# Kernel tuning notes

Measured on AMD Instinct MI355X. Metric: run time of the kernel, lower is better.

The kernel has to match this reference:

```python
import jax, jax.numpy as jnp
import numpy as np
from jax import lax

C = 64      # embed_dim
DI = 128    # d_inner (expand=2)
N = 16      # d_state
RK = 4      # dt_rank = ceil(C/16)
K = 4       # scan directions
NB = 8      # total VSS blocks (4 stages x 2)


def conv2d(x, w, b, stride=1, pad=1, groups=1):
    y = lax.conv_general_dilated(x, w, (stride, stride), [(pad, pad), (pad, pad)],
                                 dimension_numbers=('NCHW', 'OIHW', 'NCHW'),
                                 feature_group_count=groups)
    return y + b[None, :, None, None]


def ln2d(x, g, b, eps=1e-6):
    xt = x.transpose(0, 2, 3, 1)
    mu = xt.mean(-1, keepdims=True)
    var = ((xt - mu) ** 2).mean(-1, keepdims=True)
    y = (xt - mu) / jnp.sqrt(var + eps) * g + b
    return y.transpose(0, 3, 1, 2)


def selective_scan(u, delta, A, Bm, Cm, D):
    # u, delta: (B,K,d,L); A: (K,d,n); Bm, Cm: (B,K,n,L); D: (K,d)
    dA = jnp.exp(delta[..., None] * A[None, :, :, None, :])               # (B,K,d,L,n)
    dBu = delta[..., None] * Bm.transpose(0, 1, 3, 2)[:, :, None] * u[..., None]

    def comb(c1, c2):
        a1, b1 = c1
        a2, b2 = c2
        return a2 * a1, a2 * b1 + b2

    _, h = lax.associative_scan(comb, (dA, dBu), axis=3)                  # (B,K,d,L,n)
    y = jnp.einsum('bkdln,bkln->bkdl', h, Cm.transpose(0, 1, 3, 2))
    return y + D[None, :, :, None] * u


def vss_block(x, lg, lb, inw, cw, cb, xpw, dtw, dtb, a_log, dp, ong, onb, outw):
    B, _, H, W = x.shape
    L = H * W
    h = ln2d(x, lg, lb)
    xz = jnp.einsum('bchw,ce->behw', h, inw)                              # (B,2*DI,H,W)
    xc, z = xz[:, :DI], xz[:, DI:]
    xc = jax.nn.silu(conv2d(xc, cw, cb, groups=DI))                       # depthwise 3x3
    x1 = xc.reshape(B, DI, L)                                             # row-major
    x2 = xc.transpose(0, 1, 3, 2).reshape(B, DI, L)                       # col-major
    xs = jnp.stack([x1, x2, x1[..., ::-1], x2[..., ::-1]], axis=1)        # (B,K,DI,L)
    xdbl = jnp.einsum('bkdl,krd->bkrl', xs, xpw)
    dts, Bs, Cs = xdbl[:, :, :RK], xdbl[:, :, RK:RK + N], xdbl[:, :, RK + N:]
    delta = jax.nn.softplus(jnp.einsum('bkrl,kdr->bkdl', dts, dtw) + dtb[None, :, :, None])
    A = -jnp.exp(a_log)
    ys = selective_scan(xs, delta, A, Bs, Cs, dp)                         # (B,K,DI,L)
    y = (ys[:, 0].reshape(B, DI, H, W)
         + ys[:, 1].reshape(B, DI, W, H).transpose(0, 1, 3, 2)
         + ys[:, 2, :, ::-1].reshape(B, DI, H, W)
         + ys[:, 3, :, ::-1].reshape(B, DI, W, H).transpose(0, 1, 3, 2))
    yt = y.transpose(0, 2, 3, 1)
    mu = yt.mean(-1, keepdims=True)
    var = ((yt - mu) ** 2).mean(-1, keepdims=True)
    yt = (yt - mu) / jnp.sqrt(var + 1e-6) * ong + onb
    yt = yt * jax.nn.silu(z.transpose(0, 2, 3, 1))
    out = jnp.einsum('bhwd,dc->bhwc', yt, outw).transpose(0, 3, 1, 2)
    return x + out


def setup_inputs() -> dict:
    key = jax.random.key(0)
    ks = jax.random.split(key, 16)
    nrm = lambda k, s, sc=0.02: jax.random.normal(k, s, jnp.float32) * sc
    return dict(
        E0=jax.random.uniform(ks[0], (1, 1, 256, 256), jnp.float32),
        pe_w=nrm(ks[1], (C, 1, 4, 4), 0.1),
        pe_b=jnp.zeros((C,), jnp.float32),
        pe_lg=jnp.ones((C,), jnp.float32),
        pe_lb=jnp.zeros((C,), jnp.float32),
        ln_g=jnp.ones((NB, C), jnp.float32),
        ln_b=jnp.zeros((NB, C), jnp.float32),
        in_w=nrm(ks[2], (NB, C, 2 * DI)),
        cv_w=nrm(ks[3], (NB, DI, 1, 3, 3), 0.1),
        cv_b=jnp.zeros((NB, DI), jnp.float32),
        xp_w=nrm(ks[4], (NB, K, RK + 2 * N, DI)),
        dt_w=nrm(ks[5], (NB, K, DI, RK)),
        dt_b=nrm(ks[6], (NB, K, DI), 0.5),
        A_log=jnp.broadcast_to(jnp.log(jnp.arange(1., N + 1)), (NB, K, DI, N)).astype(jnp.float32),
        Dp=jnp.ones((NB, K, DI), jnp.float32),
        on_g=jnp.ones((NB, DI), jnp.float32),
        on_b=jnp.zeros((NB, DI), jnp.float32),
        out_pw=nrm(ks[7], (NB, DI, C)),
        dn_w=nrm(ks[8], (3, C, C, 3, 3), 0.05),
        dn_b=jnp.zeros((3, C), jnp.float32),
        dn_g=jnp.ones((3, C), jnp.float32),
        dn_lb=jnp.zeros((3, C), jnp.float32),
        up_w=nrm(ks[9], (3, C, C, 3, 3), 0.05),
        up_b=jnp.zeros((3, C), jnp.float32),
        oc_w=nrm(ks[10], (C, C, 3, 3), 0.05),
        oc_b=jnp.zeros((C,), jnp.float32),
    )


def reference(E0, pe_w, pe_b, pe_lg, pe_lb, ln_g, ln_b, in_w, cv_w, cv_b, xp_w,
              dt_w, dt_b, A_log, Dp, on_g, on_b, out_pw, dn_w, dn_b, dn_g, dn_lb,
              up_w, up_b, oc_w, oc_b):
    x = conv2d(E0, pe_w, pe_b, stride=4, pad=0)
    x = ln2d(x, pe_lg, pe_lb)
    skips = []
    cur = 0
    for i in range(4):
        for _ in range(2):
            x = vss_block(x, ln_g[cur], ln_b[cur], in_w[cur], cv_w[cur], cv_b[cur],
                          xp_w[cur], dt_w[cur], dt_b[cur], A_log[cur], Dp[cur],
                          on_g[cur], on_b[cur], out_pw[cur])
            cur += 1
        skips.append(x)
        if i < 3:
            x = ln2d(conv2d(x, dn_w[i], dn_b[i], stride=2), dn_g[i], dn_lb[i])
    for i in range(3):
        Bq, Cq, Hq, Wq = x.shape
        x = jax.image.resize(x, (Bq, Cq, Hq * 2, Wq * 2), method='bilinear')
        x = jax.nn.silu(conv2d(x, up_w[i], up_b[i]))
        x = x + skips[-(i + 2)]
    Bq, Cq, Hq, Wq = x.shape
    x = jax.image.resize(x, (Bq, Cq, Hq * 4, Wq * 4), method='bilinear')
    x = jax.nn.silu(conv2d(x, oc_w, oc_b))
    return x
```

## Files before the change

kernel.cpp:

```cpp
#include <hip/hip_runtime.h>
#include <hip/hip_bf16.h>
#include <utility>

__global__ void k_patch_embed_ln(const float* __restrict__ E0, const float* __restrict__ w,
                                 const float* __restrict__ b, const float* __restrict__ g,
                                 const float* __restrict__ lb, float* __restrict__ out) {
  int p = blockIdx.x;
  int c = threadIdx.x;
  int oh = p >> 6, ow = p & 63;
  const float* src = E0 + (oh * 4) * 256 + ow * 4;
  const float* wc = w + c * 16;
  float acc = b[c];
#pragma unroll
  for (int i = 0; i < 4; i++)
#pragma unroll
    for (int j = 0; j < 4; j++) acc += src[i * 256 + j] * wc[i * 4 + j];
  float s = acc, s2 = acc * acc;
#pragma unroll
  for (int m = 32; m >= 1; m >>= 1) {
    s += __shfl_xor(s, m, 64);
    s2 += __shfl_xor(s2, m, 64);
  }
  float mu = s * (1.f / 64.f);
  float var = s2 * (1.f / 64.f) - mu * mu;
  float rstd = rsqrtf(var + 1e-6f);
  out[c * 4096 + p] = (acc - mu) * rstd * g[c] + lb[c];
}

__global__ void k_ln2d64(const float* __restrict__ x, const float* __restrict__ g,
                         const float* __restrict__ b, float* __restrict__ y, int HW) {
  int p = blockIdx.x;
  int c = threadIdx.x;
  float v = x[c * HW + p];
  float s = v, s2 = v * v;
#pragma unroll
  for (int m = 32; m >= 1; m >>= 1) {
    s += __shfl_xor(s, m, 64);
    s2 += __shfl_xor(s2, m, 64);
  }
  float mu = s * (1.f / 64.f);
  float var = s2 * (1.f / 64.f) - mu * mu;
  float rstd = rsqrtf(var + 1e-6f);
  y[c * HW + p] = (v - mu) * rstd * g[c] + b[c];
}

__global__ void k_lnproj(const float* __restrict__ x, const float* __restrict__ g,
                         const float* __restrict__ b, const float* __restrict__ w,
                         float* __restrict__ xc, float* __restrict__ z, int HW) {
  int p = blockIdx.x;
  int t = threadIdx.x;
  __shared__ float hsh[64];
  if (t < 64) {
    float v = x[t * HW + p];
    float s = v, s2 = v * v;
#pragma unroll
    for (int m = 32; m >= 1; m >>= 1) {
      s += __shfl_xor(s, m, 64);
      s2 += __shfl_xor(s2, m, 64);
    }
    float mu = s * (1.f / 64.f);
    float var = s2 * (1.f / 64.f) - mu * mu;
    float rstd = rsqrtf(var + 1e-6f);
    hsh[t] = (v - mu) * rstd * g[t] + b[t];
  }
  __syncthreads();
  float acc = 0.f;
  const float* wp = w + t;
#pragma unroll
  for (int c = 0; c < 64; c++) acc += hsh[c] * wp[c * 256];
  if (t < 128)
    xc[(size_t)p * 128 + t] = acc;
  else
    z[(size_t)p * 128 + (t - 128)] = acc;
}

__global__ void k_dwconv(const float* __restrict__ xc, const float* __restrict__ w,
                         const float* __restrict__ b, float* __restrict__ out, int H, int lgH) {
  int HW = H * H;
  int idx = blockIdx.x * blockDim.x + threadIdx.x;
  if (idx >= 32 * HW) return;
  int p = idx >> 5;
  int d0 = (idx & 31) * 4;
  int ph = p >> lgH, pw = p & (H - 1);
  float4 acc = *(const float4*)(b + d0);
#pragma unroll
  for (int i = 0; i < 3; i++) {
    int ih = ph + i - 1;
    if (ih < 0 || ih >= H) continue;
#pragma unroll
    for (int j = 0; j < 3; j++) {
      int iw = pw + j - 1;
      if (iw < 0 || iw >= H) continue;
      float4 xv = *(const float4*)(xc + (size_t)(ih * H + iw) * 128 + d0);
      int tap = i * 3 + j;
      acc.x += xv.x * w[(d0 + 0) * 9 + tap];
      acc.y += xv.y * w[(d0 + 1) * 9 + tap];
      acc.z += xv.z * w[(d0 + 2) * 9 + tap];
      acc.w += xv.w * w[(d0 + 3) * 9 + tap];
    }
  }
  float4 o;
  o.x = acc.x / (1.f + __expf(-acc.x));
  o.y = acc.y / (1.f + __expf(-acc.y));
  o.z = acc.z / (1.f + __expf(-acc.z));
  o.w = acc.w / (1.f + __expf(-acc.w));
  *(float4*)(out + (size_t)p * 128 + d0) = o;
}

__global__ void __launch_bounds__(256) k_xproj_scanA(
    const float* __restrict__ xcs, const float* __restrict__ xpw,
    const float* __restrict__ dtw, const float* __restrict__ dtb,
    const float* __restrict__ A_log, float* __restrict__ delta, float* __restrict__ Bs,
    float* __restrict__ Cs, float* __restrict__ hloc, float* __restrict__ pA, int H,
    int lgH, int nc, int cs) {
  extern __shared__ float smem[];
  float* xs = smem;
  float* dsh = xs + cs * 128;
  float* Bsh = dsh + cs * 128;
  float* r4s = Bsh + cs * 16;
  int L = H * H;
  int c = blockIdx.x;
  int k = blockIdx.y;
  int t = threadIdx.x;
  int l0 = c * cs;
  for (int i = t; i < cs * 128; i += 256) {
    int j = i >> 7, d = i & 127;
    int l = l0 + j;
    int lm = (k & 2) ? (L - 1 - l) : l;
    int idx = (k & 1) ? ((lm & (H - 1)) * H + (lm >> lgH)) : lm;
    xs[j * 128 + d] = xcs[(size_t)idx * 128 + d];
  }
  int r = t >> 2, q = t & 3;
  float4 wreg[8];
  if (t < 144) {
    const float4* wp = (const float4*)(xpw + (size_t)(k * 36 + r) * 128 + q * 32);
#pragma unroll
    for (int m = 0; m < 8; m++) wreg[m] = wp[m];
  }
  float4 dtw4 = {0, 0, 0, 0};
  float dtbv = 0.f;
  if (t < 128) {
    dtw4 = *(const float4*)(dtw + (size_t)(k * 128 + t) * 4);
    dtbv = dtb[k * 128 + t];
  }
  __syncthreads();
  for (int j = 0; j < cs; j++) {
    if (t < 144) {
      const float4* xp = (const float4*)&xs[j * 128 + q * 32];
      float a = 0.f;
#pragma unroll
      for (int m = 0; m < 8; m++) {
        float4 xv = xp[m];
        a += xv.x * wreg[m].x + xv.y * wreg[m].y + xv.z * wreg[m].z + xv.w * wreg[m].w;
      }
      a += __shfl_xor(a, 1);
      a += __shfl_xor(a, 2);
      if (q == 0) {
        int l = l0 + j;
        if (r < 4)
          r4s[r] = a;
        else if (r < 20) {
          Bsh[j * 16 + (r - 4)] = a;
          Bs[((size_t)k * L + l) * 16 + (r - 4)] = a;
        } else
          Cs[((size_t)k * L + l) * 16 + (r - 20)] = a;
      }
    }
    __syncthreads();
    if (t < 128) {
      float dt = dtbv + r4s[0] * dtw4.x + r4s[1] * dtw4.y + r4s[2] * dtw4.z + r4s[3] * dtw4.w;
      float sp = fmaxf(dt, 0.f) + log1pf(__expf(-fabsf(dt)));
      dsh[j * 128 + t] = sp;
      delta[((size_t)k * L + (l0 + j)) * 128 + t] = sp;
    }
    __syncthreads();
  }
  if (t < 128) {
    int d = t;
    float A[16], h[16];
#pragma unroll
    for (int n = 0; n < 16; n++) {
      A[n] = -__expf(A_log[(size_t)(k * 128 + d) * 16 + n]);
      h[n] = 0.f;
    }
    float sumdt = 0.f;
    for (int j = 0; j < cs; j++) {
      float u = xs[j * 128 + d];
      float dt = dsh[j * 128 + d];
      float du = dt * u;
      sumdt += dt;
      const float4* bp = (const float4*)&Bsh[j * 16];
      float4 B0 = bp[0], B1 = bp[1], B2 = bp[2], B3 = bp[3];
      float Bv[16] = {B0.x, B0.y, B0.z, B0.w, B1.x, B1.y, B1.z, B1.w,
                      B2.x, B2.y, B2.z, B2.w, B3.x, B3.y, B3.z, B3.w};
#pragma unroll
      for (int n = 0; n < 16; n++) h[n] = __expf(dt * A[n]) * h[n] + Bv[n] * du;
    }
    size_t base = (((size_t)(k * 128 + d)) * nc + c) * 16;
#pragma unroll
    for (int n = 0; n < 16; n++) {
      hloc[base + n] = h[n];
      pA[base + n] = __expf(A[n] * sumdt);
    }
  }
}

__global__ void k_scanB(const float* __restrict__ hloc, const float* __restrict__ pA,
                        float* __restrict__ hinit, int nc) {
  int tid = blockIdx.x * blockDim.x + threadIdx.x;
  int k = tid >> 11;
  int d = (tid >> 4) & 127;
  int n = tid & 15;
  size_t rb = ((size_t)(k * 128 + d)) * nc * 16 + n;
  float h = 0.f;
  for (int c = 0; c < nc; c++) {
    size_t a = rb + (size_t)c * 16;
    hinit[a] = h;
    h = pA[a] * h + hloc[a];
  }
}

__global__ void k_scanC(const float* __restrict__ xcs, const float* __restrict__ delta,
                        const float* __restrict__ Bs, const float* __restrict__ Cs,
                        const float* __restrict__ A_log, const float* __restrict__ Dp,
                        const float* __restrict__ hloc, const float* __restrict__ pA,
                        const float* __restrict__ hinit, float* __restrict__ ys, int H,
                        int lgH, int nc, int cs, int ipref) {
  int L = H * H;
  int c = blockIdx.x;
  int k = blockIdx.y;
  int d = threadIdx.x;
  float A[16], h[16];
  size_t rb = ((size_t)(k * 128 + d)) * nc * 16;
#pragma unroll
  for (int n = 0; n < 16; n++) A[n] = -__expf(A_log[(size_t)(k * 128 + d) * 16 + n]);
  if (ipref) {
#pragma unroll
    for (int n = 0; n < 16; n++) h[n] = 0.f;
    for (int cc = 0; cc < c; cc++) {
      const float4* pp = (const float4*)(pA + rb + (size_t)cc * 16);
      const float4* hh = (const float4*)(hloc + rb + (size_t)cc * 16);
      float4 P0 = pp[0], P1 = pp[1], P2 = pp[2], P3 = pp[3];
      float4 Q0 = hh[0], Q1 = hh[1], Q2 = hh[2], Q3 = hh[3];
      h[0] = P0.x * h[0] + Q0.x;  h[1] = P0.y * h[1] + Q0.y;
      h[2] = P0.z * h[2] + Q0.z;  h[3] = P0.w * h[3] + Q0.w;
      h[4] = P1.x * h[4] + Q1.x;  h[5] = P1.y * h[5] + Q1.y;
      h[6] = P1.z * h[6] + Q1.z;  h[7] = P1.w * h[7] + Q1.w;
      h[8] = P2.x * h[8] + Q2.x;  h[9] = P2.y * h[9] + Q2.y;
      h[10] = P2.z * h[10] + Q2.z; h[11] = P2.w * h[11] + Q2.w;
      h[12] = P3.x * h[12] + Q3.x; h[13] = P3.y * h[13] + Q3.y;
      h[14] = P3.z * h[14] + Q3.z; h[15] = P3.w * h[15] + Q3.w;
    }
  } else {
#pragma unroll
    for (int n = 0; n < 16; n++) h[n] = hinit[rb + (size_t)c * 16 + n];
  }
  float Dv = Dp[k * 128 + d];
  int l0 = c * cs;
  for (int l = l0; l < l0 + cs; l++) {
    int lm = (k & 2) ? (L - 1 - l) : l;
    int idx = (k & 1) ? ((lm & (H - 1)) * H + (lm >> lgH)) : lm;
    float u = xcs[(size_t)idx * 128 + d];
    float dt = delta[((size_t)k * L + l) * 128 + d];
    float du = dt * u;
    const float4* bp = (const float4*)(Bs + ((size_t)k * L + l) * 16);
    float4 B0 = bp[0], B1 = bp[1], B2 = bp[2], B3 = bp[3];
    float Bv[16] = {B0.x, B0.y, B0.z, B0.w, B1.x, B1.y, B1.z, B1.w,
                    B2.x, B2.y, B2.z, B2.w, B3.x, B3.y, B3.z, B3.w};
    const float4* cp = (const float4*)(Cs + ((size_t)k * L + l) * 16);
    float4 C0 = cp[0], C1 = cp[1], C2 = cp[2], C3 = cp[3];
    float Cv[16] = {C0.x, C0.y, C0.z, C0.w, C1.x, C1.y, C1.z, C1.w,
                    C2.x, C2.y, C2.z, C2.w, C3.x, C3.y, C3.z, C3.w};
    float y = 0.f;
#pragma unroll
    for (int n = 0; n < 16; n++) {
      h[n] = __expf(dt * A[n]) * h[n] + Bv[n] * du;
      y += h[n] * Cv[n];
    }
    ys[((size_t)k * L + l) * 128 + d] = y + Dv * u;
  }
}

__global__ void k_combine(const float* __restrict__ ys, const float* __restrict__ z,
                          const float* __restrict__ xin, const float* __restrict__ ong,
                          const float* __restrict__ onb, const float* __restrict__ outw,
                          float* __restrict__ xout, int H, int lgH) {
  int L = H * H;
  int p = blockIdx.x;
  int d = threadIdx.x;
  int ph = p >> lgH, pw = p & (H - 1);
  int l1 = pw * H + ph;
  float yv = ys[((size_t)0 * L + p) * 128 + d] + ys[((size_t)1 * L + l1) * 128 + d] +
             ys[((size_t)2 * L + (L - 1 - p)) * 128 + d] +
             ys[((size_t)3 * L + (L - 1 - l1)) * 128 + d];
  float s = yv, s2 = yv * yv;
#pragma unroll
  for (int m = 32; m >= 1; m >>= 1) {
    s += __shfl_xor(s, m, 64);
    s2 += __shfl_xor(s2, m, 64);
  }
  __shared__ float ws1[2], ws2[2];
  int wid = d >> 6;
  if ((d & 63) == 0) {
    ws1[wid] = s;
    ws2[wid] = s2;
  }
  __syncthreads();
  float tot = ws1[0] + ws1[1], tot2 = ws2[0] + ws2[1];
  float mu = tot * (1.f / 128.f);
  float var = tot2 * (1.f / 128.f) - mu * mu;
  float rstd = rsqrtf(var + 1e-6f);
  float zt = z[(size_t)p * 128 + d];
  float yt = ((yv - mu) * rstd * ong[d] + onb[d]) * (zt / (1.f + __expf(-zt)));
  __shared__ float ysm[128];
  ysm[d] = yt;
  __syncthreads();
  if (d < 64) {
    float acc = xin[(size_t)d * L + p];
#pragma unroll
    for (int q = 0; q < 128; q++) acc += ysm[q] * outw[q * 64 + d];
    xout[(size_t)d * L + p] = acc;
  }
}

__global__ void k_combine_lnproj(const float* __restrict__ ys, const float* __restrict__ z,
                                 const float* __restrict__ xin, const float* __restrict__ ong,
                                 const float* __restrict__ onb, const float* __restrict__ outw,
                                 const float* __restrict__ g2, const float* __restrict__ b2,
                                 const float* __restrict__ w2, float* __restrict__ xout,
                                 float* __restrict__ xc, float* __restrict__ zout, int H,
                                 int lgH) {
  int L = H * H;
  int p = blockIdx.x;
  int t = threadIdx.x;
  __shared__ float ysm[128], hnsh[64];
  __shared__ float ws1[2], ws2[2];
  float yv = 0.f;
  if (t < 128) {
    int ph = p >> lgH, pw = p & (H - 1);
    int l1 = pw * H + ph;
    yv = ys[((size_t)0 * L + p) * 128 + t] + ys[((size_t)1 * L + l1) * 128 + t] +
         ys[((size_t)2 * L + (L - 1 - p)) * 128 + t] +
         ys[((size_t)3 * L + (L - 1 - l1)) * 128 + t];
    float s = yv, s2 = yv * yv;
#pragma unroll
    for (int m = 32; m >= 1; m >>= 1) {
      s += __shfl_xor(s, m, 64);
      s2 += __shfl_xor(s2, m, 64);
    }
    if ((t & 63) == 0) {
      ws1[t >> 6] = s;
      ws2[t >> 6] = s2;
    }
  }
  __syncthreads();
  if (t < 128) {
    float tot = ws1[0] + ws1[1], tot2 = ws2[0] + ws2[1];
    float mu = tot * (1.f / 128.f);
    float var = tot2 * (1.f / 128.f) - mu * mu;
    float rstd = rsqrtf(var + 1e-6f);
    float zt = z[(size_t)p * 128 + t];
    ysm[t] = ((yv - mu) * rstd * ong[t] + onb[t]) * (zt / (1.f + __expf(-zt)));
  }
  __syncthreads();
  if (t < 64) {
    float acc = xin[(size_t)t * L + p];
#pragma unroll
    for (int q = 0; q < 128; q++) acc += ysm[q] * outw[q * 64 + t];
    xout[(size_t)t * L + p] = acc;
    float s = acc, s2 = acc * acc;
#pragma unroll
    for (int m = 32; m >= 1; m >>= 1) {
      s += __shfl_xor(s, m, 64);
      s2 += __shfl_xor(s2, m, 64);
    }
    float mu = s * (1.f / 64.f);
    float var = s2 * (1.f / 64.f) - mu * mu;
    float rstd = rsqrtf(var + 1e-6f);
    hnsh[t] = (acc - mu) * rstd * g2[t] + b2[t];
  }
  __syncthreads();
  float a2 = 0.f;
  const float* wp = w2 + t;
#pragma unroll
  for (int c = 0; c < 64; c++) a2 += hnsh[c] * wp[c * 256];
  if (t < 128)
    xc[(size_t)p * 128 + t] = a2;
  else
    zout[(size_t)p * 128 + (t - 128)] = a2;
}

__global__ void k_conv_naive(const float* __restrict__ x, const float* __restrict__ w,
                             const float* __restrict__ b, const float* __restrict__ skip,
                             float* __restrict__ out, int Hin, int Hout, int stride,
                             int do_silu) {
  int idx = blockIdx.x * blockDim.x + threadIdx.x;
  int HWo = Hout * Hout;
  if (idx >= 64 * HWo) return;
  int co = idx / HWo;
  int p = idx - co * HWo;
  int oh = p / Hout, ow = p - (p / Hout) * Hout;
  float acc = b[co];
  const float* wb = w + co * 64 * 9;
  for (int ci = 0; ci < 64; ci++) {
    const float* xb = x + (size_t)ci * Hin * Hin;
    const float* wc = wb + ci * 9;
#pragma unroll
    for (int i = 0; i < 3; i++) {
      int ih = oh * stride + i - 1;
      if (ih < 0 || ih >= Hin) continue;
#pragma unroll
      for (int j = 0; j < 3; j++) {
        int iw = ow * stride + j - 1;
        if (iw < 0 || iw >= Hin) continue;
        acc += xb[ih * Hin + iw] * wc[i * 3 + j];
      }
    }
  }
  if (do_silu) acc = acc / (1.f + __expf(-acc));
  if (skip) acc += skip[idx];
  out[idx] = acc;
}

__global__ void k_phase_weights(const float* __restrict__ w, float* __restrict__ Wp) {
  int co = blockIdx.x;
  int ph = blockIdx.y;
  int ci = threadIdx.x;
  int py = ph >> 2, px = ph & 3;
  float ay[3][3], ax[3][3];
#pragma unroll
  for (int d = 0; d < 3; d++)
#pragma unroll
    for (int s = 0; s < 3; s++) {
      ay[d][s] = 0.f;
      ax[d][s] = 0.f;
    }
#pragma unroll
  for (int d = 0; d < 3; d++) {
    {
      float tt = (py + d - 1) * 0.25f - 0.375f;
      float e = floorf(tt);
      float f = tt - e;
      int ei = (int)e;
#pragma unroll
      for (int s = 0; s < 3; s++) {
        if (s == ei + 1) ay[d][s] += 1.f - f;
        if (s == ei + 2) ay[d][s] += f;
      }
    }
    {
      float tt = (px + d - 1) * 0.25f - 0.375f;
      float e = floorf(tt);
      float f = tt - e;
      int ei = (int)e;
#pragma unroll
      for (int s = 0; s < 3; s++) {
        if (s == ei + 1) ax[d][s] += 1.f - f;
        if (s == ei + 2) ax[d][s] += f;
      }
    }
  }
  const float* wc = w + ((size_t)co * 64 + ci) * 9;
  float wv[9];
#pragma unroll
  for (int i = 0; i < 9; i++) wv[i] = wc[i];
  float* dst = Wp + (((size_t)ph * 64 + co) * 64 + ci) * 9;
#pragma unroll
  for (int sy = 0; sy < 3; sy++)
#pragma unroll
    for (int sx = 0; sx < 3; sx++) {
      float a = 0.f;
#pragma unroll
      for (int dy = 0; dy < 3; dy++)
#pragma unroll
        for (int dx = 0; dx < 3; dx++) a += wv[dy * 3 + dx] * ay[dy][sy] * ax[dx][sx];
      dst[sy * 3 + sx] = a;
    }
}

__global__ void __launch_bounds__(256) k_conv_phase(const float* __restrict__ x,
                                                    const float* __restrict__ Wp,
                                                    const float* __restrict__ bias,
                                                    float* __restrict__ out) {
  __shared__ __align__(16) float ssh[8][18][20];
  __shared__ __align__(16) float wsh[8][16][12];
  int t = threadIdx.x;
  int q = t & 63, cg = t >> 6;
  int qx = q & 7, qy = q >> 3;
  int tx = blockIdx.x & 3, ty = blockIdx.x >> 2;
  int ph = blockIdx.y;
  int py = ph >> 2, px = ph & 3;
  int z16 = blockIdx.z * 16;
  int by = ty * 16, bx = tx * 16;
  float acc[4][4];
#pragma unroll
  for (int pp = 0; pp < 4; pp++)
#pragma unroll
    for (int i = 0; i < 4; i++) acc[pp][i] = 0.f;
  for (int cb = 0; cb < 64; cb += 8) {
    for (int i = t; i < 8 * 324; i += 256) {
      int ci = i / 324;
      int rr = i - ci * 324;
      int ry = rr / 18, rx = rr - ry * 18;
      int sy = min(max(by + ry - 1, 0), 63);
      int sx = min(max(bx + rx - 1, 0), 63);
      ssh[ci][ry][rx] = x[(size_t)(cb + ci) * 4096 + sy * 64 + sx];
    }
    for (int i = t; i < 8 * 144; i += 256) {
      int ci = i / 144;
      int rr = i - ci * 144;
      int col = rr / 9, tap = rr - col * 9;
      wsh[ci][col][tap] = Wp[(((size_t)ph * 64 + z16 + col) * 64 + cb + ci) * 9 + tap];
    }
    __syncthreads();
#pragma unroll 2
    for (int ci = 0; ci < 8; ci++) {
      float xv[4][4];
#pragma unroll
      for (int r = 0; r < 4; r++) {
        float2 a = *(const float2*)&ssh[ci][2 * qy + r][2 * qx];
        float2 bq = *(const float2*)&ssh[ci][2 * qy + r][2 * qx + 2];
        xv[r][0] = a.x;
        xv[r][1] = a.y;
        xv[r][2] = bq.x;
        xv[r][3] = bq.y;
      }
#pragma unroll
      for (int i = 0; i < 4; i++) {
        int col = cg * 4 + i;
        float4 w0 = *(const float4*)&wsh[ci][col][0];
        float4 w1 = *(const float4*)&wsh[ci][col][4];
        float w8 = wsh[ci][col][8];
#pragma unroll
        for (int dr = 0; dr < 2; dr++)
#pragma unroll
          for (int dc = 0; dc < 2; dc++) {
            acc[dr * 2 + dc][i] += xv[dr + 0][dc + 0] * w0.x + xv[dr + 0][dc + 1] * w0.y +
                                   xv[dr + 0][dc + 2] * w0.z + xv[dr + 1][dc + 0] * w0.w +
                                   xv[dr + 1][dc + 1] * w1.x + xv[dr + 1][dc + 2] * w1.y +
                                   xv[dr + 2][dc + 0] * w1.z + xv[dr + 2][dc + 1] * w1.w +
                                   xv[dr + 2][dc + 2] * w8;
          }
      }
    }
    __syncthreads();
  }
#pragma unroll
  for (int dr = 0; dr < 2; dr++)
#pragma unroll
    for (int dc = 0; dc < 2; dc++) {
      int sy = by + 2 * qy + dr, sx = bx + 2 * qx + dc;
      int gy = 4 * sy + py, gx = 4 * sx + px;
#pragma unroll
      for (int i = 0; i < 4; i++) {
        int co = z16 + cg * 4 + i;
        float a = acc[dr * 2 + dc][i] + bias[co];
        a = a / (1.f + __expf(-a));
        out[(size_t)co * 65536 + gy * 256 + gx] = a;
      }
    }
}

__global__ void k_final_ring(const float* __restrict__ x, const float* __restrict__ w,
                             const float* __restrict__ b, float* __restrict__ out) {
  int tid = blockIdx.x * blockDim.x + threadIdx.x;
  if (tid >= 1020 * 64) return;
  int co = tid & 63;
  int pix = tid >> 6;
  int gy, gx;
  if (pix < 256) {
    gy = 0;
    gx = pix;
  } else if (pix < 512) {
    gy = 255;
    gx = pix - 256;
  } else if (pix < 766) {
    gy = pix - 512 + 1;
    gx = 0;
  } else {
    gy = pix - 766 + 1;
    gx = 255;
  }
  float fh[3], fw[3];
  int y0[3], y1[3], x0[3], x1[3];
  bool vy[3], vx[3];
#pragma unroll
  for (int d = 0; d < 3; d++) {
    int g = gy + d - 1;
    vy[d] = (g >= 0 && g < 256);
    float s = g * 0.25f - 0.375f;
    float e = floorf(s);
    int ei = (int)e;
    fh[d] = s - e;
    y0[d] = min(max(ei, 0), 63);
    y1[d] = min(max(ei + 1, 0), 63);
    g = gx + d - 1;
    vx[d] = (g >= 0 && g < 256);
    s = g * 0.25f - 0.375f;
    e = floorf(s);
    ei = (int)e;
    fw[d] = s - e;
    x0[d] = min(max(ei, 0), 63);
    x1[d] = min(max(ei + 1, 0), 63);
  }
  const float* wb = w + (size_t)co * 576;
  float acc = b[co];
  for (int ci = 0; ci < 64; ci++) {
    const float* xb = x + (size_t)ci * 4096;
    const float* wc = wb + ci * 9;
#pragma unroll
    for (int dy = 0; dy < 3; dy++) {
      if (!vy[dy]) continue;
#pragma unroll
      for (int dx = 0; dx < 3; dx++) {
        if (!vx[dx]) continue;
        float u = (1.f - fh[dy]) * ((1.f - fw[dx]) * xb[y0[dy] * 64 + x0[dx]] +
                                    fw[dx] * xb[y0[dy] * 64 + x1[dx]]) +
                  fh[dy] * ((1.f - fw[dx]) * xb[y1[dy] * 64 + x0[dx]] +
                            fw[dx] * xb[y1[dy] * 64 + x1[dx]]);
        acc += wc[dy * 3 + dx] * u;
      }
    }
  }
  acc = acc / (1.f + __expf(-acc));
  out[(size_t)co * 65536 + gy * 256 + gx] = acc;
}

__global__ void k_resize(const float* __restrict__ x, float* __restrict__ out, int Hin,
                         int Win, int Hout, int Wout, float inv_scale) {
  int idx = blockIdx.x * blockDim.x + threadIdx.x;
  int HWo = Hout * Wout;
  if (idx >= 64 * HWo) return;
  int c = idx / HWo;
  int p = idx - c * HWo;
  int oh = p / Wout, ow = p - (p / Wout) * Wout;
  float sh = (oh + 0.5f) * inv_scale - 0.5f;
  float sw = (ow + 0.5f) * inv_scale - 0.5f;
  int h0 = (int)floorf(sh);
  float fh = sh - h0;
  int w0 = (int)floorf(sw);
  float fw = sw - w0;
  int h0c = min(max(h0, 0), Hin - 1), h1c = min(max(h0 + 1, 0), Hin - 1);
  int w0c = min(max(w0, 0), Win - 1), w1c = min(max(w0 + 1, 0), Win - 1);
  const float* xb = x + (size_t)c * Hin * Win;
  float v = (1.f - fh) * ((1.f - fw) * xb[h0c * Win + w0c] + fw * xb[h0c * Win + w1c]) +
            fh * ((1.f - fw) * xb[h1c * Win + w0c] + fw * xb[h1c * Win + w1c]);
  out[idx] = v;
}

extern "C" void kernel_launch(void* const* d_in, const int* in_sizes, int n_in, void* d_out,
                              int out_size, void* d_ws, size_t ws_size, hipStream_t stream) {
  const float* E0 = (const float*)d_in[0];
  const float* pe_w = (const float*)d_in[1];
  const float* pe_b = (const float*)d_in[2];
  const float* pe_lg = (const float*)d_in[3];
  const float* pe_lb = (const float*)d_in[4];
  const float* ln_g = (const float*)d_in[5];
  const float* ln_b = (const float*)d_in[6];
  const float* in_w = (const float*)d_in[7];
  const float* cv_w = (const float*)d_in[8];
  const float* cv_b = (const float*)d_in[9];
  const float* xp_w = (const float*)d_in[10];
  const float* dt_w = (const float*)d_in[11];
  const float* dt_b = (const float*)d_in[12];
  const float* A_log = (const float*)d_in[13];
  const float* Dp = (const float*)d_in[14];
  const float* on_g = (const float*)d_in[15];
  const float* on_b = (const float*)d_in[16];
  const float* out_pw = (const float*)d_in[17];
  const float* dn_w = (const float*)d_in[18];
  const float* dn_b = (const float*)d_in[19];
  const float* dn_g = (const float*)d_in[20];
  const float* dn_lb = (const float*)d_in[21];
  const float* up_w = (const float*)d_in[22];
  const float* up_b = (const float*)d_in[23];
  const float* oc_w = (const float*)d_in[24];
  const float* oc_b = (const float*)d_in[25];

  float* ws = (float*)d_ws;
  size_t off = 0;
  auto alloc = [&](size_t n) {
    float* p = ws + off;
    off += n;
    return p;
  };
  float* xA = alloc(64 * 4096);
  float* xB = alloc(64 * 4096);
  float* xc = alloc(128 * 4096);
  float* zb = alloc(128 * 4096);
  float* xcs = alloc(128 * 4096);
  float* dlt = alloc((size_t)4 * 128 * 4096);
  float* Bsb = alloc(4 * 16 * 4096);
  float* Csb = alloc(4 * 16 * 4096);
  float* ysb = alloc((size_t)4 * 128 * 4096);
  float* hloc = alloc((size_t)4 * 128 * 128 * 16);
  float* pAb = alloc((size_t)4 * 128 * 128 * 16);
  float* hin = alloc((size_t)4 * 128 * 128 * 16);
  float* sk0 = alloc(64 * 4096);
  float* sk1 = alloc(64 * 1024);
  float* sk2 = alloc(64 * 256);
  float* sk3 = alloc(64 * 64);
  float* tmpR = alloc((size_t)64 * 4096);
  float* Wpb = alloc((size_t)16 * 64 * 64 * 9);

  k_phase_weights<<<dim3(64, 16), 64, 0, stream>>>(oc_w, Wpb);

  k_patch_embed_ln<<<4096, 64, 0, stream>>>(E0, pe_w, pe_b, pe_lg, pe_lb, xB);
  float* x = xB;
  float* xalt = xA;

  int Hs[4] = {64, 32, 16, 8};
  int lgHs[4] = {6, 5, 4, 3};
  int CSs[4] = {32, 16, 8, 8};
  float* skips[4] = {sk0, sk1, sk2, sk3};
  int cur = 0;

  auto vss_core = [&](int H, int lgH, int cs) {
    int L = H * H;
    int nc = L / cs;
    k_dwconv<<<(32 * L + 255) / 256, 256, 0, stream>>>(xc, cv_w + (size_t)cur * 128 * 9,
                                                       cv_b + cur * 128, xcs, H, lgH);
    const float* Al = A_log + (size_t)cur * 4 * 128 * 16;
    const float* Dv = Dp + cur * 4 * 128;
    dim3 ga(nc, 4);
    size_t shb = (size_t)(cs * 128 * 2 + cs * 16 + 4) * sizeof(float);
    k_xproj_scanA<<<ga, 256, shb, stream>>>(xcs, xp_w + (size_t)cur * 4 * 36 * 128,
                                            dt_w + (size_t)cur * 4 * 128 * 4,
                                            dt_b + cur * 4 * 128, Al, dlt, Bsb, Csb, hloc,
                                            pAb, H, lgH, nc, cs);
    int ipref = (nc <= 32) ? 1 : 0;
    if (!ipref) k_scanB<<<32, 256, 0, stream>>>(hloc, pAb, hin, nc);
    dim3 gc(nc, 4);
    k_scanC<<<gc, 128, 0, stream>>>(xcs, dlt, Bsb, Csb, Al, Dv, hloc, pAb, hin, ysb, H,
                                    lgH, nc, cs, ipref);
  };

  for (int i = 0; i < 4; i++) {
    int H = Hs[i], lgH = lgHs[i];
    int L = H * H;
    k_lnproj<<<L, 256, 0, stream>>>(x, ln_g + cur * 64, ln_b + cur * 64,
                                    in_w + (size_t)cur * 64 * 256, xc, zb, L);
    vss_core(H, lgH, CSs[i]);
    k_combine_lnproj<<<L, 256, 0, stream>>>(
        ysb, zb, x, on_g + cur * 128, on_b + cur * 128, out_pw + (size_t)cur * 128 * 64,
        ln_g + (cur + 1) * 64, ln_b + (cur + 1) * 64, in_w + (size_t)(cur + 1) * 64 * 256,
        xalt, xc, zb, H, lgH);
    std::swap(x, xalt);
    cur++;
    vss_core(H, lgH, CSs[i]);
    if (i < 3) {
      k_combine<<<L, 128, 0, stream>>>(ysb, zb, x, on_g + cur * 128, on_b + cur * 128,
                                       out_pw + (size_t)cur * 128 * 64, skips[i], H, lgH);
      cur++;
      int Ho = H / 2;
      k_conv_naive<<<(64 * Ho * Ho + 255) / 256, 256, 0, stream>>>(
          skips[i], dn_w + (size_t)i * 64 * 64 * 9, dn_b + i * 64, nullptr, xalt, H, Ho, 2, 0);
      k_ln2d64<<<Ho * Ho, 64, 0, stream>>>(xalt, dn_g + i * 64, dn_lb + i * 64, x, Ho * Ho);
    } else {
      k_combine<<<L, 128, 0, stream>>>(ysb, zb, x, on_g + cur * 128, on_b + cur * 128,
                                       out_pw + (size_t)cur * 128 * 64, xalt, H, lgH);
      std::swap(x, xalt);
      cur++;
    }
  }

  for (int i = 0; i < 3; i++) {
    int Hin = 8 << i, Ho = Hin * 2;
    k_resize<<<(64 * Ho * Ho + 255) / 256, 256, 0, stream>>>(x, tmpR, Hin, Hin, Ho, Ho, 0.5f);
    k_conv_naive<<<(64 * Ho * Ho + 255) / 256, 256, 0, stream>>>(
        tmpR, up_w + (size_t)i * 64 * 64 * 9, up_b + i * 64, skips[2 - i], xalt, Ho, Ho, 1, 1);
    std::swap(x, xalt);
  }

  dim3 gp(16, 16, 4);
  k_conv_phase<<<gp, 256, 0, stream>>>(x, Wpb, oc_b, (float*)d_out);
  k_final_ring<<<255, 256, 0, stream>>>(x, oc_w, oc_b, (float*)d_out);
}
```

Before: 1.306 ms.

## Fuse LN stages into in-projection, drop scanB, split final conv over more blocks

Patch-embed+LN and downsample-LN are each fused with the following block's LN and in-projection, which removes two launches and one activation round trip per stage. The separate chunk-prefix scan kernel is removed and every scanC block always recomputes its prefix serially. For stage 0 that means up to 128 chunks of serial prefix work per block. The final phase conv now computes 8 output channels per block instead of 16, which doubles the grid for more parallelism but reloads the input tile more often.

```diff
diff --git a/kernel.cpp b/kernel.cpp
--- a/kernel.cpp
+++ b/kernel.cpp
@@ -2,57 +2,25 @@
 #include <hip/hip_bf16.h>
 #include <utility>
 
-__global__ void k_patch_embed_ln(const float* __restrict__ E0, const float* __restrict__ w,
-                                 const float* __restrict__ b, const float* __restrict__ g,
-                                 const float* __restrict__ lb, float* __restrict__ out) {
-  int p = blockIdx.x;
-  int c = threadIdx.x;
-  int oh = p >> 6, ow = p & 63;
-  const float* src = E0 + (oh * 4) * 256 + ow * 4;
-  const float* wc = w + c * 16;
-  float acc = b[c];
-#pragma unroll
-  for (int i = 0; i < 4; i++)
-#pragma unroll
-    for (int j = 0; j < 4; j++) acc += src[i * 256 + j] * wc[i * 4 + j];
-  float s = acc, s2 = acc * acc;
-#pragma unroll
-  for (int m = 32; m >= 1; m >>= 1) {
-    s += __shfl_xor(s, m, 64);
-    s2 += __shfl_xor(s2, m, 64);
-  }
-  float mu = s * (1.f / 64.f);
-  float var = s2 * (1.f / 64.f) - mu * mu;
-  float rstd = rsqrtf(var + 1e-6f);
-  out[c * 4096 + p] = (acc - mu) * rstd * g[c] + lb[c];
-}
-
-__global__ void k_ln2d64(const float* __restrict__ x, const float* __restrict__ g,
-                         const float* __restrict__ b, float* __restrict__ y, int HW) {
-  int p = blockIdx.x;
-  int c = threadIdx.x;
-  float v = x[c * HW + p];
-  float s = v, s2 = v * v;
-#pragma unroll
-  for (int m = 32; m >= 1; m >>= 1) {
-    s += __shfl_xor(s, m, 64);
-    s2 += __shfl_xor(s2, m, 64);
-  }
-  float mu = s * (1.f / 64.f);
-  float var = s2 * (1.f / 64.f) - mu * mu;
-  float rstd = rsqrtf(var + 1e-6f);
-  y[c * HW + p] = (v - mu) * rstd * g[c] + b[c];
-}
-
-__global__ void k_lnproj(const float* __restrict__ x, const float* __restrict__ g,
-                         const float* __restrict__ b, const float* __restrict__ w,
-                         float* __restrict__ xc, float* __restrict__ z, int HW) {
+__global__ void k_pe_lnproj(const float* __restrict__ E0, const float* __restrict__ w,
+                            const float* __restrict__ b, const float* __restrict__ g1,
+                            const float* __restrict__ b1, const float* __restrict__ g2,
+                            const float* __restrict__ b2, const float* __restrict__ w2,
+                            float* __restrict__ xres, float* __restrict__ xc,
+                            float* __restrict__ z) {
   int p = blockIdx.x;
   int t = threadIdx.x;
   __shared__ float hsh[64];
   if (t < 64) {
-    float v = x[t * HW + p];
-    float s = v, s2 = v * v;
+    int oh = p >> 6, ow = p & 63;
+    const float* src = E0 + (oh * 4) * 256 + ow * 4;
+    const float* wc = w + t * 16;
+    float acc = b[t];
+#pragma unroll
+    for (int i = 0; i < 4; i++)
+#pragma unroll
+      for (int j = 0; j < 4; j++) acc += src[i * 256 + j] * wc[i * 4 + j];
+    float s = acc, s2 = acc * acc;
 #pragma unroll
     for (int m = 32; m >= 1; m >>= 1) {
       s += __shfl_xor(s, m, 64);
@@ -60,12 +28,64 @@
     }
     float mu = s * (1.f / 64.f);
     float var = s2 * (1.f / 64.f) - mu * mu;
-    float rstd = rsqrtf(var + 1e-6f);
-    hsh[t] = (v - mu) * rstd * g[t] + b[t];
+    float v1 = (acc - mu) * rsqrtf(var + 1e-6f) * g1[t] + b1[t];
+    xres[t * 4096 + p] = v1;
+    s = v1;
+    s2 = v1 * v1;
+#pragma unroll
+    for (int m = 32; m >= 1; m >>= 1) {
+      s += __shfl_xor(s, m, 64);
+      s2 += __shfl_xor(s2, m, 64);
+    }
+    mu = s * (1.f / 64.f);
+    var = s2 * (1.f / 64.f) - mu * mu;
+    hsh[t] = (v1 - mu) * rsqrtf(var + 1e-6f) * g2[t] + b2[t];
   }
   __syncthreads();
   float acc = 0.f;
-  const float* wp = w + t;
+  const float* wp = w2 + t;
+#pragma unroll
+  for (int c = 0; c < 64; c++) acc += hsh[c] * wp[c * 256];
+  if (t < 128)
+    xc[(size_t)p * 128 + t] = acc;
+  else
+    z[(size_t)p * 128 + (t - 128)] = acc;
+}
+
+__global__ void k_dnln_lnproj(const float* __restrict__ cv, const float* __restrict__ g1,
+                              const float* __restrict__ b1, const float* __restrict__ g2,
+                              const float* __restrict__ b2, const float* __restrict__ w2,
+                              float* __restrict__ xres, float* __restrict__ xc,
+                              float* __restrict__ z, int HW) {
+  int p = blockIdx.x;
+  int t = threadIdx.x;
+  __shared__ float hsh[64];
+  if (t < 64) {
+    float v = cv[t * HW + p];
+    float s = v, s2 = v * v;
+#pragma unroll
+    for (int m = 32; m >= 1; m >>= 1) {
+      s += __shfl_xor(s, m, 64);
+      s2 += __shfl_xor(s2, m, 64);
+    }
+    float mu = s * (1.f / 64.f);
+    float var = s2 * (1.f / 64.f) - mu * mu;
+    float v1 = (v - mu) * rsqrtf(var + 1e-6f) * g1[t] + b1[t];
+    xres[t * HW + p] = v1;
+    s = v1;
+    s2 = v1 * v1;
+#pragma unroll
+    for (int m = 32; m >= 1; m >>= 1) {
+      s += __shfl_xor(s, m, 64);
+      s2 += __shfl_xor(s2, m, 64);
+    }
+    mu = s * (1.f / 64.f);
+    var = s2 * (1.f / 64.f) - mu * mu;
+    hsh[t] = (v1 - mu) * rsqrtf(var + 1e-6f) * g2[t] + b2[t];
+  }
+  __syncthreads();
+  float acc = 0.f;
+  const float* wp = w2 + t;
 #pragma unroll
   for (int c = 0; c < 64; c++) acc += hsh[c] * wp[c * 256];
   if (t < 128)
@@ -205,27 +225,11 @@
   }
 }
 
-__global__ void k_scanB(const float* __restrict__ hloc, const float* __restrict__ pA,
-                        float* __restrict__ hinit, int nc) {
-  int tid = blockIdx.x * blockDim.x + threadIdx.x;
-  int k = tid >> 11;
-  int d = (tid >> 4) & 127;
-  int n = tid & 15;
-  size_t rb = ((size_t)(k * 128 + d)) * nc * 16 + n;
-  float h = 0.f;
-  for (int c = 0; c < nc; c++) {
-    size_t a = rb + (size_t)c * 16;
-    hinit[a] = h;
-    h = pA[a] * h + hloc[a];
-  }
-}
-
 __global__ void k_scanC(const float* __restrict__ xcs, const float* __restrict__ delta,
                         const float* __restrict__ Bs, const float* __restrict__ Cs,
                         const float* __restrict__ A_log, const float* __restrict__ Dp,
                         const float* __restrict__ hloc, const float* __restrict__ pA,
-                        const float* __restrict__ hinit, float* __restrict__ ys, int H,
-                        int lgH, int nc, int cs, int ipref) {
+                        float* __restrict__ ys, int H, int lgH, int nc, int cs) {
   int L = H * H;
   int c = blockIdx.x;
   int k = blockIdx.y;
@@ -233,27 +237,23 @@
   float A[16], h[16];
   size_t rb = ((size_t)(k * 128 + d)) * nc * 16;
 #pragma unroll
-  for (int n = 0; n < 16; n++) A[n] = -__expf(A_log[(size_t)(k * 128 + d) * 16 + n]);
-  if (ipref) {
-#pragma unroll
-    for (int n = 0; n < 16; n++) h[n] = 0.f;
-    for (int cc = 0; cc < c; cc++) {
-      const float4* pp = (const float4*)(pA + rb + (size_t)cc * 16);
-      const float4* hh = (const float4*)(hloc + rb + (size_t)cc * 16);
-      float4 P0 = pp[0], P1 = pp[1], P2 = pp[2], P3 = pp[3];
-      float4 Q0 = hh[0], Q1 = hh[1], Q2 = hh[2], Q3 = hh[3];
-      h[0] = P0.x * h[0] + Q0.x;  h[1] = P0.y * h[1] + Q0.y;
-      h[2] = P0.z * h[2] + Q0.z;  h[3] = P0.w * h[3] + Q0.w;
-      h[4] = P1.x * h[4] + Q1.x;  h[5] = P1.y * h[5] + Q1.y;
-      h[6] = P1.z * h[6] + Q1.z;  h[7] = P1.w * h[7] + Q1.w;
-      h[8] = P2.x * h[8] + Q2.x;  h[9] = P2.y * h[9] + Q2.y;
-      h[10] = P2.z * h[10] + Q2.z; h[11] = P2.w * h[11] + Q2.w;
-      h[12] = P3.x * h[12] + Q3.x; h[13] = P3.y * h[13] + Q3.y;
-      h[14] = P3.z * h[14] + Q3.z; h[15] = P3.w * h[15] + Q3.w;
-    }
-  } else {
-#pragma unroll
-    for (int n = 0; n < 16; n++) h[n] = hinit[rb + (size_t)c * 16 + n];
+  for (int n = 0; n < 16; n++) {
+    A[n] = -__expf(A_log[(size_t)(k * 128 + d) * 16 + n]);
+    h[n] = 0.f;
+  }
+  for (int cc = 0; cc < c; cc++) {
+    const float4* pp = (const float4*)(pA + rb + (size_t)cc * 16);
+    const float4* hh = (const float4*)(hloc + rb + (size_t)cc * 16);
+    float4 P0 = pp[0], P1 = pp[1], P2 = pp[2], P3 = pp[3];
+    float4 Q0 = hh[0], Q1 = hh[1], Q2 = hh[2], Q3 = hh[3];
+    h[0] = P0.x * h[0] + Q0.x;   h[1] = P0.y * h[1] + Q0.y;
+    h[2] = P0.z * h[2] + Q0.z;   h[3] = P0.w * h[3] + Q0.w;
+    h[4] = P1.x * h[4] + Q1.x;   h[5] = P1.y * h[5] + Q1.y;
+    h[6] = P1.z * h[6] + Q1.z;   h[7] = P1.w * h[7] + Q1.w;
+    h[8] = P2.x * h[8] + Q2.x;   h[9] = P2.y * h[9] + Q2.y;
+    h[10] = P2.z * h[10] + Q2.z; h[11] = P2.w * h[11] + Q2.w;
+    h[12] = P3.x * h[12] + Q3.x; h[13] = P3.y * h[13] + Q3.y;
+    h[14] = P3.z * h[14] + Q3.z; h[15] = P3.w * h[15] + Q3.w;
   }
   float Dv = Dp[k * 128 + d];
   int l0 = c * cs;
@@ -483,20 +483,20 @@
                                                     const float* __restrict__ bias,
                                                     float* __restrict__ out) {
   __shared__ __align__(16) float ssh[8][18][20];
-  __shared__ __align__(16) float wsh[8][16][12];
+  __shared__ __align__(16) float wsh[8][8][12];
   int t = threadIdx.x;
   int q = t & 63, cg = t >> 6;
   int qx = q & 7, qy = q >> 3;
   int tx = blockIdx.x & 3, ty = blockIdx.x >> 2;
   int ph = blockIdx.y;
   int py = ph >> 2, px = ph & 3;
-  int z16 = blockIdx.z * 16;
+  int z8 = blockIdx.z * 8;
   int by = ty * 16, bx = tx * 16;
-  float acc[4][4];
+  float acc[4][2];
 #pragma unroll
   for (int pp = 0; pp < 4; pp++)
 #pragma unroll
-    for (int i = 0; i < 4; i++) acc[pp][i] = 0.f;
+    for (int i = 0; i < 2; i++) acc[pp][i] = 0.f;
   for (int cb = 0; cb < 64; cb += 8) {
     for (int i = t; i < 8 * 324; i += 256) {
       int ci = i / 324;
@@ -506,11 +506,11 @@
       int sx = min(max(bx + rx - 1, 0), 63);
       ssh[ci][ry][rx] = x[(size_t)(cb + ci) * 4096 + sy * 64 + sx];
     }
-    for (int i = t; i < 8 * 144; i += 256) {
-      int ci = i / 144;
-      int rr = i - ci * 144;
+    for (int i = t; i < 8 * 72; i += 256) {
+      int ci = i / 72;
+      int rr = i - ci * 72;
       int col = rr / 9, tap = rr - col * 9;
-      wsh[ci][col][tap] = Wp[(((size_t)ph * 64 + z16 + col) * 64 + cb + ci) * 9 + tap];
+      wsh[ci][col][tap] = Wp[(((size_t)ph * 64 + z8 + col) * 64 + cb + ci) * 9 + tap];
     }
     __syncthreads();
 #pragma unroll 2
@@ -526,8 +526,8 @@
         xv[r][3] = bq.y;
       }
 #pragma unroll
-      for (int i = 0; i < 4; i++) {
-        int col = cg * 4 + i;
+      for (int i = 0; i < 2; i++) {
+        int col = cg * 2 + i;
         float4 w0 = *(const float4*)&wsh[ci][col][0];
         float4 w1 = *(const float4*)&wsh[ci][col][4];
         float w8 = wsh[ci][col][8];
@@ -552,8 +552,8 @@
       int sy = by + 2 * qy + dr, sx = bx + 2 * qx + dc;
       int gy = 4 * sy + py, gx = 4 * sx + px;
 #pragma unroll
-      for (int i = 0; i < 4; i++) {
-        int co = z16 + cg * 4 + i;
+      for (int i = 0; i < 2; i++) {
+        int co = z8 + cg * 2 + i;
         float a = acc[dr * 2 + dc][i] + bias[co];
         a = a / (1.f + __expf(-a));
         out[(size_t)co * 65536 + gy * 256 + gx] = a;
@@ -695,7 +695,6 @@
   float* ysb = alloc((size_t)4 * 128 * 4096);
   float* hloc = alloc((size_t)4 * 128 * 128 * 16);
   float* pAb = alloc((size_t)4 * 128 * 128 * 16);
-  float* hin = alloc((size_t)4 * 128 * 128 * 16);
   float* sk0 = alloc(64 * 4096);
   float* sk1 = alloc(64 * 1024);
   float* sk2 = alloc(64 * 256);
@@ -705,9 +704,11 @@
 
   k_phase_weights<<<dim3(64, 16), 64, 0, stream>>>(oc_w, Wpb);
 
-  k_patch_embed_ln<<<4096, 64, 0, stream>>>(E0, pe_w, pe_b, pe_lg, pe_lb, xB);
   float* x = xB;
   float* xalt = xA;
+
+  k_pe_lnproj<<<4096, 256, 0, stream>>>(E0, pe_w, pe_b, pe_lg, pe_lb, ln_g, ln_b, in_w, x,
+                                        xc, zb);
 
   int Hs[4] = {64, 32, 16, 8};
   int lgHs[4] = {6, 5, 4, 3};
@@ -728,18 +729,14 @@
                                             dt_w + (size_t)cur * 4 * 128 * 4,
                                             dt_b + cur * 4 * 128, Al, dlt, Bsb, Csb, hloc,
                                             pAb, H, lgH, nc, cs);
-    int ipref = (nc <= 32) ? 1 : 0;
-    if (!ipref) k_scanB<<<32, 256, 0, stream>>>(hloc, pAb, hin, nc);
     dim3 gc(nc, 4);
-    k_scanC<<<gc, 128, 0, stream>>>(xcs, dlt, Bsb, Csb, Al, Dv, hloc, pAb, hin, ysb, H,
-                                    lgH, nc, cs, ipref);
+    k_scanC<<<gc, 128, 0, stream>>>(xcs, dlt, Bsb, Csb, Al, Dv, hloc, pAb, ysb, H, lgH, nc,
+                                    cs);
   };
 
   for (int i = 0; i < 4; i++) {
     int H = Hs[i], lgH = lgHs[i];
     int L = H * H;
-    k_lnproj<<<L, 256, 0, stream>>>(x, ln_g + cur * 64, ln_b + cur * 64,
-                                    in_w + (size_t)cur * 64 * 256, xc, zb, L);
     vss_core(H, lgH, CSs[i]);
     k_combine_lnproj<<<L, 256, 0, stream>>>(
         ysb, zb, x, on_g + cur * 128, on_b + cur * 128, out_pw + (size_t)cur * 128 * 64,
@@ -754,8 +751,11 @@
       cur++;
       int Ho = H / 2;
       k_conv_naive<<<(64 * Ho * Ho + 255) / 256, 256, 0, stream>>>(
-          skips[i], dn_w + (size_t)i * 64 * 64 * 9, dn_b + i * 64, nullptr, xalt, H, Ho, 2, 0);
-      k_ln2d64<<<Ho * Ho, 64, 0, stream>>>(xalt, dn_g + i * 64, dn_lb + i * 64, x, Ho * Ho);
+          skips[i], dn_w + (size_t)i * 64 * 64 * 9, dn_b + i * 64, nullptr, tmpR, H, Ho, 2, 0);
+      k_dnln_lnproj<<<Ho * Ho, 256, 0, stream>>>(tmpR, dn_g + i * 64, dn_lb + i * 64,
+                                                 ln_g + cur * 64, ln_b + cur * 64,
+                                                 in_w + (size_t)cur * 64 * 256, x, xc, zb,
+                                                 Ho * Ho);
     } else {
       k_combine<<<L, 128, 0, stream>>>(ysb, zb, x, on_g + cur * 128, on_b + cur * 128,
                                        out_pw + (size_t)cur * 128 * 64, xalt, H, lgH);
@@ -772,7 +772,7 @@
     std::swap(x, xalt);
   }
 
-  dim3 gp(16, 16, 4);
+  dim3 gp(16, 16, 8);
   k_conv_phase<<<gp, 256, 0, stream>>>(x, Wpb, oc_b, (float*)d_out);
   k_final_ring<<<255, 256, 0, stream>>>(x, oc_w, oc_b, (float*)d_out);
 }
```

After: 1.523 ms. +16.6%, slower.
